# Kernel optimization log

Hardware: AMD Instinct MI355X
Metric: run time of the kernel (lower is better)

The kernel has to match this reference:

```python
import jax, jax.numpy as jnp
import numpy as np

EMBED_DIM = 1024
NUM_HEADS = 16
HEAD_DIM = EMBED_DIM // NUM_HEADS


def setup_inputs() -> dict:
    key = jax.random.key(0)
    ks = jax.random.split(key, 5)
    x = jax.random.normal(ks[0], (2, 2048, EMBED_DIM), dtype=jnp.float32)
    s_in = 1.0 / np.sqrt(EMBED_DIM)
    W_qkv = jax.random.uniform(ks[1], (EMBED_DIM, 3 * EMBED_DIM), minval=-s_in, maxval=s_in, dtype=jnp.float32)
    b_qkv = jax.random.uniform(ks[2], (3 * EMBED_DIM,), minval=-s_in, maxval=s_in, dtype=jnp.float32)
    W_out = jax.random.uniform(ks[3], (EMBED_DIM, EMBED_DIM), minval=-s_in, maxval=s_in, dtype=jnp.float32)
    b_out = jax.random.uniform(ks[4], (EMBED_DIM,), minval=-s_in, maxval=s_in, dtype=jnp.float32)
    return {"x": x, "W_qkv": W_qkv, "b_qkv": b_qkv, "W_out": W_out, "b_out": b_out}


def reference(x, W_qkv, b_qkv, W_out, b_out):
    B, S, D = x.shape
    H, Dh = NUM_HEADS, HEAD_DIM
    qkv = x @ W_qkv + b_qkv                       # [B, S, 3D]
    q, k, v = jnp.split(qkv, 3, axis=-1)
    # [B, S, D] -> [B, H, S, Dh]
    q = q.reshape(B, S, H, Dh).transpose(0, 2, 1, 3)
    k = k.reshape(B, S, H, Dh).transpose(0, 2, 1, 3)
    v = v.reshape(B, S, H, Dh).transpose(0, 2, 1, 3)
    scores = jnp.einsum('bhqd,bhkd->bhqk', q, k) / jnp.sqrt(jnp.float32(Dh))
    probs = jax.nn.softmax(scores, axis=-1)       # [B, H, S, S]
    attn = jnp.einsum('bhqk,bhkd->bhqd', probs, v)
    attn = attn.transpose(0, 2, 1, 3).reshape(B, S, D)
    return attn @ W_out + b_out
```

## Files before the change

kernel.cpp:

```cpp
#include <hip/hip_runtime.h>
#include <hip/hip_bf16.h>

#define DEV __device__ __forceinline__

typedef __bf16 bf16x8 __attribute__((ext_vector_type(8)));
typedef float f32x4 __attribute__((ext_vector_type(4)));
typedef float f32x16 __attribute__((ext_vector_type(16)));
using u16 = unsigned short;
using u32 = unsigned int;

static constexpr int S = 2048;
static constexpr int D = 1024;
static constexpr float SCQ = 0.125f * 1.44269504088896340736f;

DEV u16 f2bf(float f) {
  unsigned u = __builtin_bit_cast(unsigned, f);
  u += 0x7fffu + ((u >> 16) & 1u);
  return (u16)(u >> 16);
}
DEV u16 f2bfr(float f) {
  return (u16)((__builtin_bit_cast(u32, f) + 0x8000u) >> 16);
}
DEV u32 pk2(float a, float b) {
  u32 ua = __builtin_bit_cast(u32, a) + 0x8000u;
  u32 ub = __builtin_bit_cast(u32, b) + 0x8000u;
  return __builtin_amdgcn_perm(ub, ua, 0x07060302);
}

DEV void gl16(const u16* __restrict__ g, u16* l) {
  __builtin_amdgcn_global_load_lds((const __attribute__((address_space(1))) u32*)g,
                                   (__attribute__((address_space(3))) u32*)l, 16, 0, 0);
}

__global__ __launch_bounds__(256) void k_prep(const float* __restrict__ x, u16* __restrict__ Xb,
                                              const float* __restrict__ Wqkv, u16* __restrict__ WqkvT,
                                              const float* __restrict__ Wout, u16* __restrict__ WoutT) {
  __shared__ float t[32][33];
  const int bid = blockIdx.x;
  const int tid = threadIdx.x;
  if (bid < 4096) {
    const int i = bid * 256 + tid;
    const float4 v = reinterpret_cast<const float4*>(x)[i];
    ushort4 o;
    o.x = f2bf(v.x); o.y = f2bf(v.y); o.z = f2bf(v.z); o.w = f2bf(v.w);
    reinterpret_cast<ushort4*>(Xb)[i] = o;
    return;
  }
  const float* in;
  u16* out;
  int R, C, bx, by;
  if (bid < 4096 + 3072) {
    const int b = bid - 4096;
    in = Wqkv; out = WqkvT; R = 1024; C = 3072;
    bx = b % 96; by = b / 96;
  } else {
    const int b = bid - 7168;
    in = Wout; out = WoutT; R = 1024; C = 1024;
    bx = b & 31; by = b >> 5;
  }
  const int tx = tid & 31, ty = tid >> 5;
  const int c0 = bx * 32, r0 = by * 32;
  for (int i = ty; i < 32; i += 8)
    t[i][tx] = in[(size_t)(r0 + i) * C + c0 + tx];
  __syncthreads();
  for (int i = ty; i < 32; i += 8)
    out[(size_t)(c0 + i) * R + r0 + tx] = f2bf(t[tx][i]);
}

__global__ __launch_bounds__(256, 5) void k_gemm0(const u16* __restrict__ A, const u16* __restrict__ Bt,
                                                  const float* __restrict__ bias, int M, int N, int K,
                                                  u16* __restrict__ Qb, u16* __restrict__ Kb,
                                                  u16* __restrict__ Vt) {
  constexpr int TN = 128, NJ = 4;
  constexpr int ASZ = 2 * 128 * 32 * 2;
  __shared__ __align__(16) char smem[ASZ + 2 * TN * 32 * 2];
  auto As = reinterpret_cast<u16(*)[128][32]>(smem);
  auto Bs = reinterpret_cast<u16(*)[TN][32]>(smem + ASZ);
  auto LT = reinterpret_cast<u16(*)[136]>(smem);
  const int tid = threadIdx.x;
  const int lane = tid & 63, wave = tid >> 6;
  const int l15 = lane & 15, quad = lane >> 4;
  const int m0 = blockIdx.y * 128, n0 = blockIdx.x * TN;
  const int wm = (wave >> 1) * 64, wn = (wave & 1) * (TN / 2);
  const int lr = lane >> 2;
  const int lcs = ((((lane & 3) - (lane >> 3)) & 3)) * 8;
  const int sq = ((quad + (l15 >> 1)) & 3) * 8;

  f32x4 acc[4][NJ];
#pragma unroll
  for (int i = 0; i < 4; i++)
#pragma unroll
    for (int j = 0; j < NJ; j++) acc[i][j] = (f32x4){0.f, 0.f, 0.f, 0.f};

  const u16* Aw0 = &A[(size_t)(m0 + wave * 32 + lr) * K + lcs];
  const u16* Aw1 = &A[(size_t)(m0 + wave * 32 + 16 + lr) * K + lcs];
  const u16* Bw0 = &Bt[(size_t)(n0 + wave * 32 + lr) * K + lcs];
  const u16* Bw1 = &Bt[(size_t)(n0 + wave * 32 + 16 + lr) * K + lcs];

  gl16(Aw0, &As[0][wave * 32][0]);
  gl16(Aw1, &As[0][wave * 32 + 16][0]);
  gl16(Bw0, &Bs[0][wave * 32][0]);
  gl16(Bw1, &Bs[0][wave * 32 + 16][0]);

  int cur = 0;
#pragma unroll 2
  for (int kk = 0; kk < K; kk += 32, cur ^= 1) {
    __syncthreads();
    if (kk + 32 < K) {
      gl16(Aw0 + kk + 32, &As[cur ^ 1][wave * 32][0]);
      gl16(Aw1 + kk + 32, &As[cur ^ 1][wave * 32 + 16][0]);
      gl16(Bw0 + kk + 32, &Bs[cur ^ 1][wave * 32][0]);
      gl16(Bw1 + kk + 32, &Bs[cur ^ 1][wave * 32 + 16][0]);
    }
    bf16x8 af[4], bfv[NJ];
#pragma unroll
    for (int i = 0; i < 4; i++)
      af[i] = *reinterpret_cast<const bf16x8*>(&As[cur][wm + i * 16 + l15][sq]);
#pragma unroll
    for (int j = 0; j < NJ; j++)
      bfv[j] = *reinterpret_cast<const bf16x8*>(&Bs[cur][wn + j * 16 + l15][sq]);
#pragma unroll
    for (int i = 0; i < 4; i++)
#pragma unroll
      for (int j = 0; j < NJ; j++)
        acc[i][j] = __builtin_amdgcn_mfma_f32_16x16x32_bf16(af[i], bfv[j], acc[i][j], 0, 0, 0);
  }

  if (n0 >= 2048) {
    const int b = m0 >> 11, sbase = m0 & 2047;
#pragma unroll
    for (int p = 0; p < 2; p++) {
      __syncthreads();
      if ((wave & 1) == p) {
#pragma unroll
        for (int j = 0; j < NJ; j++) {
          const int n = n0 + wn + j * 16 + l15;
          const float vb = bias[n];
#pragma unroll
          for (int i = 0; i < 4; i++) {
            uint2 pw;
            pw.x = pk2(acc[i][j][0] + vb, acc[i][j][1] + vb);
            pw.y = pk2(acc[i][j][2] + vb, acc[i][j][3] + vb);
            *reinterpret_cast<uint2*>(&LT[j * 16 + l15][wm + i * 16 + quad * 4]) = pw;
          }
        }
      }
      __syncthreads();
      const int h = ((n0 - 2048) >> 6) + p;
      const int bh = b * 16 + h;
      const int nl = tid >> 2, cc = (tid & 3) * 32;
      u16* dst = &Vt[((size_t)bh * 64 + nl) * S + sbase + cc];
#pragma unroll
      for (int k = 0; k < 4; k++)
        reinterpret_cast<uint4*>(dst)[k] = *reinterpret_cast<const uint4*>(&LT[nl][cc + k * 8]);
    }
  } else {
#pragma unroll
    for (int i = 0; i < 4; i++) {
#pragma unroll
      for (int j = 0; j < NJ; j++) {
#pragma unroll
        for (int r = 0; r < 4; r++) {
          const int m = m0 + wm + i * 16 + quad * 4 + r;
          const int n = n0 + wn + j * 16 + l15;
          const float v = acc[i][j][r] + bias[n];
          const int h = (n >> 6) & 15, dh = n & 63;
          const int b = m >> 11, s = m & 2047;
          const int bh = b * 16 + h;
          if (n < 1024) Qb[((size_t)bh * S + s) * 64 + dh] = f2bfr(v * SCQ);
          else          Kb[((size_t)bh * S + s) * 64 + dh] = f2bfr(v);
        }
      }
    }
  }
}

__global__ __launch_bounds__(256, 4) void k_gemm2(const u16* __restrict__ A, const u16* __restrict__ Bt,
                                                  const float* __restrict__ bias, float* __restrict__ outF) {
  constexpr int K = 1024, N = 1024;
  __shared__ __align__(16) u16 As[2][64][64];
  __shared__ __align__(16) u16 Bs[2][64][64];
  const int tid = threadIdx.x;
  const int lane = tid & 63, wave = tid >> 6;
  const int l15 = lane & 15, quad = lane >> 4;
  const int m0 = blockIdx.y * 64, n0 = blockIdx.x * 64;
  const int wm = (wave >> 1) * 32, wn = (wave & 1) * 32;
  const int srow = lane >> 3;
  const int scol = ((lane & 7) ^ srow) * 8;

  f32x4 acc[2][2];
#pragma unroll
  for (int i = 0; i < 2; i++)
#pragma unroll
    for (int j = 0; j < 2; j++) acc[i][j] = (f32x4){0.f, 0.f, 0.f, 0.f};

  const u16* Ap[2];
  const u16* Bp[2];
#pragma unroll
  for (int c = 0; c < 2; c++) {
    Ap[c] = &A[(size_t)(m0 + wave * 16 + c * 8 + srow) * K + scol];
    Bp[c] = &Bt[(size_t)(n0 + wave * 16 + c * 8 + srow) * K + scol];
  }

#pragma unroll
  for (int c = 0; c < 2; c++) {
    gl16(Ap[c], &As[0][wave * 16 + c * 8][0]);
    gl16(Bp[c], &Bs[0][wave * 16 + c * 8][0]);
  }

  int cur = 0;
#pragma unroll 2
  for (int kk = 0; kk < K; kk += 64, cur ^= 1) {
    __syncthreads();
    if (kk + 64 < K) {
#pragma unroll
      for (int c = 0; c < 2; c++) {
        gl16(Ap[c] + kk + 64, &As[cur ^ 1][wave * 16 + c * 8][0]);
        gl16(Bp[c] + kk + 64, &Bs[cur ^ 1][wave * 16 + c * 8][0]);
      }
    }
#pragma unroll
    for (int ks = 0; ks < 2; ks++) {
      const int sc = ((ks * 4 + quad) ^ (l15 & 7)) * 8;
      bf16x8 af[2], bfv[2];
#pragma unroll
      for (int i = 0; i < 2; i++)
        af[i] = *reinterpret_cast<const bf16x8*>(&As[cur][wm + i * 16 + l15][sc]);
#pragma unroll
      for (int j = 0; j < 2; j++)
        bfv[j] = *reinterpret_cast<const bf16x8*>(&Bs[cur][wn + j * 16 + l15][sc]);
#pragma unroll
      for (int i = 0; i < 2; i++)
#pragma unroll
        for (int j = 0; j < 2; j++)
          acc[i][j] = __builtin_amdgcn_mfma_f32_16x16x32_bf16(af[i], bfv[j], acc[i][j], 0, 0, 0);
    }
  }

#pragma unroll
  for (int i = 0; i < 2; i++)
#pragma unroll
    for (int j = 0; j < 2; j++)
#pragma unroll
      for (int r = 0; r < 4; r++) {
        const int m = m0 + wm + i * 16 + quad * 4 + r;
        const int n = n0 + wn + j * 16 + l15;
        outF[(size_t)m * N + n] = acc[i][j][r] + bias[n];
      }
}

__global__ __launch_bounds__(256, 2) void k_attn(const u16* __restrict__ Qb,
                                                 const u16* __restrict__ Kb,
                                                 const u16* __restrict__ Vt,
                                                 u16* __restrict__ attnB) {
  __shared__ u16 Ks[64][72];
  __shared__ u16 Vs[64][72];
  __shared__ u16 Pl[4][32][72];
  const int bh = blockIdx.y;
  const int q0 = blockIdx.x * 128;
  const int tid = threadIdx.x;
  const int lane = tid & 63, wave = tid >> 6;
  const int l31 = lane & 31, hi = lane >> 5;
  const u16* Qh = Qb + (size_t)bh * S * 64;
  const u16* Kh = Kb + (size_t)bh * S * 64;
  const u16* Vh = Vt + (size_t)bh * 64 * S;
  const int qrow = q0 + wave * 32 + l31;
  bf16x8 qf[4];
#pragma unroll
  for (int f = 0; f < 4; f++)
    qf[f] = *reinterpret_cast<const bf16x8*>(&Qh[(size_t)qrow * 64 + f * 16 + hi * 8]);

  const int r0 = tid >> 3, c0 = (tid & 7) * 8;

  float li = 0.f;
  f32x16 o0, o1;
#pragma unroll
  for (int r = 0; r < 16; r++) { o0[r] = 0.f; o1[r] = 0.f; }

  uint4 pk0 = *reinterpret_cast<const uint4*>(&Kh[(size_t)r0 * 64 + c0]);
  uint4 pk1 = *reinterpret_cast<const uint4*>(&Kh[(size_t)(r0 + 32) * 64 + c0]);
  uint4 pv0 = *reinterpret_cast<const uint4*>(&Vh[(size_t)r0 * S + c0]);
  uint4 pv1 = *reinterpret_cast<const uint4*>(&Vh[(size_t)(r0 + 32) * S + c0]);

  for (int kb = 0; kb < S / 64; kb++) {
    __syncthreads();
    *reinterpret_cast<uint4*>(&Ks[r0][c0]) = pk0;
    *reinterpret_cast<uint4*>(&Ks[r0 + 32][c0]) = pk1;
    *reinterpret_cast<uint4*>(&Vs[r0][c0]) = pv0;
    *reinterpret_cast<uint4*>(&Vs[r0 + 32][c0]) = pv1;
    __syncthreads();
    if (kb + 1 < S / 64) {
      const u16* Kn = Kh + (size_t)(kb + 1) * 64 * 64;
      pk0 = *reinterpret_cast<const uint4*>(&Kn[(size_t)r0 * 64 + c0]);
      pk1 = *reinterpret_cast<const uint4*>(&Kn[(size_t)(r0 + 32) * 64 + c0]);
      pv0 = *reinterpret_cast<const uint4*>(&Vh[(size_t)r0 * S + (kb + 1) * 64 + c0]);
      pv1 = *reinterpret_cast<const uint4*>(&Vh[(size_t)(r0 + 32) * S + (kb + 1) * 64 + c0]);
    }
    f32x16 z[2];
    __builtin_amdgcn_s_setprio(1);
#pragma unroll
    for (int kt = 0; kt < 2; kt++) {
#pragma unroll
      for (int r = 0; r < 16; r++) z[kt][r] = 0.f;
#pragma unroll
      for (int f = 0; f < 4; f++) {
        const bf16x8 a = *reinterpret_cast<const bf16x8*>(&Ks[kt * 32 + l31][f * 16 + hi * 8]);
        z[kt] = __builtin_amdgcn_mfma_f32_32x32x16_bf16(a, qf[f], z[kt], 0, 0, 0);
      }
    }
    __builtin_amdgcn_s_setprio(0);
    float s0 = 0.f, s1 = 0.f, s2 = 0.f, s3 = 0.f;
#pragma unroll
    for (int kt = 0; kt < 2; kt++)
#pragma unroll
      for (int r = 0; r < 16; r++) {
        const float p = __builtin_amdgcn_exp2f(z[kt][r]);
        z[kt][r] = p;
        if ((r & 3) == 0) s0 += p; else if ((r & 3) == 1) s1 += p;
        else if ((r & 3) == 2) s2 += p; else s3 += p;
      }
    li += (s0 + s1) + (s2 + s3);
#pragma unroll
    for (int kt = 0; kt < 2; kt++)
#pragma unroll
      for (int g = 0; g < 4; g++) {
        uint2 pw;
        pw.x = pk2(z[kt][g * 4 + 0], z[kt][g * 4 + 1]);
        pw.y = pk2(z[kt][g * 4 + 2], z[kt][g * 4 + 3]);
        *reinterpret_cast<uint2*>(&Pl[wave][l31][kt * 32 + g * 8 + hi * 4]) = pw;
      }
    __builtin_amdgcn_s_setprio(1);
#pragma unroll
    for (int f = 0; f < 4; f++) {
      const bf16x8 bp = *reinterpret_cast<const bf16x8*>(&Pl[wave][l31][f * 16 + hi * 8]);
      const bf16x8 av0 = *reinterpret_cast<const bf16x8*>(&Vs[l31][f * 16 + hi * 8]);
      const bf16x8 av1 = *reinterpret_cast<const bf16x8*>(&Vs[32 + l31][f * 16 + hi * 8]);
      o0 = __builtin_amdgcn_mfma_f32_32x32x16_bf16(av0, bp, o0, 0, 0, 0);
      o1 = __builtin_amdgcn_mfma_f32_32x32x16_bf16(av1, bp, o1, 0, 0, 0);
    }
    __builtin_amdgcn_s_setprio(0);
  }
  li += __shfl_xor(li, 32);
  const float inv = 1.f / li;
#pragma unroll
  for (int dt = 0; dt < 2; dt++) {
    const f32x16& od = dt ? o1 : o0;
#pragma unroll
    for (int g = 0; g < 4; g++) {
      uint2 ow;
      ow.x = pk2(od[g * 4 + 0] * inv, od[g * 4 + 1] * inv);
      ow.y = pk2(od[g * 4 + 2] * inv, od[g * 4 + 3] * inv);
      *reinterpret_cast<uint2*>(&Pl[wave][l31][dt * 32 + g * 8 + hi * 4]) = ow;
    }
  }
  const int b = bh >> 4, h = bh & 15;
  const int mbase = b * S + q0 + wave * 32;
  const int qr = lane >> 1, ch = (lane & 1) * 32;
  u16* dst = &attnB[(size_t)(mbase + qr) * D + h * 64 + ch];
#pragma unroll
  for (int c = 0; c < 4; c++)
    reinterpret_cast<uint4*>(dst)[c] = *reinterpret_cast<const uint4*>(&Pl[wave][qr][ch + c * 8]);
}

extern "C" void kernel_launch(void* const* d_in, const int* in_sizes, int n_in,
                              void* d_out, int out_size, void* d_ws, size_t ws_size,
                              hipStream_t stream) {
  const float* x = (const float*)d_in[0];
  const float* Wqkv = (const float*)d_in[1];
  const float* bqkv = (const float*)d_in[2];
  const float* Wout = (const float*)d_in[3];
  const float* bout = (const float*)d_in[4];
  float* out = (float*)d_out;

  char* p = (char*)d_ws;
  u16* Xb = (u16*)p;    p += (size_t)4096 * 1024 * 2;
  u16* WqkvT = (u16*)p; p += (size_t)3072 * 1024 * 2;
  u16* WoutT = (u16*)p; p += (size_t)1024 * 1024 * 2;
  u16* Qb = (u16*)p;    p += (size_t)32 * 2048 * 64 * 2;
  u16* Kb = (u16*)p;    p += (size_t)32 * 2048 * 64 * 2;
  u16* Vt = (u16*)p;    p += (size_t)32 * 64 * 2048 * 2;
  u16* attnB = (u16*)p; p += (size_t)4096 * 1024 * 2;

  k_prep<<<4096 + 3072 + 1024, 256, 0, stream>>>(x, Xb, Wqkv, WqkvT, Wout, WoutT);
  k_gemm0<<<dim3(3072 / 128, 4096 / 128), 256, 0, stream>>>(
      Xb, WqkvT, bqkv, 4096, 3072, 1024, Qb, Kb, Vt);
  k_attn<<<dim3(2048 / 128, 32), 256, 0, stream>>>(Qb, Kb, Vt, attnB);
  k_gemm2<<<dim3(1024 / 64, 4096 / 64), 256, 0, stream>>>(attnB, WoutT, bout, out);
}
```

Before: 190.3 us.

## Double attention key tile to 128 and remap block order in GEMMs and attention

The attention kernel now processes 128 keys per iteration instead of 64, which halves the number of barrier-separated loop iterations and doubles the work per synchronisation. It uses larger shared-memory K, V and P tiles, and adds a barrier before the final output staging. All three kernels also remap the linear block id so that consecutive blocks are spread across groups of 8, intended to improve L2/cache locality across XCDs. The larger LDS footprint and higher register use may reduce occupancy in the attention kernel.

```diff
diff --git a/kernel.cpp b/kernel.cpp
--- a/kernel.cpp
+++ b/kernel.cpp
@@ -80,7 +80,9 @@
   const int tid = threadIdx.x;
   const int lane = tid & 63, wave = tid >> 6;
   const int l15 = lane & 15, quad = lane >> 4;
-  const int m0 = blockIdx.y * 128, n0 = blockIdx.x * TN;
+  const int bid0 = blockIdx.x + 24 * blockIdx.y;
+  const int bid = (bid0 & 7) * 96 + (bid0 >> 3);
+  const int m0 = (bid / 24) * 128, n0 = (bid % 24) * TN;
   const int wm = (wave >> 1) * 64, wn = (wave & 1) * (TN / 2);
   const int lr = lane >> 2;
   const int lcs = ((((lane & 3) - (lane >> 3)) & 3)) * 8;
@@ -183,7 +185,9 @@
   const int tid = threadIdx.x;
   const int lane = tid & 63, wave = tid >> 6;
   const int l15 = lane & 15, quad = lane >> 4;
-  const int m0 = blockIdx.y * 64, n0 = blockIdx.x * 64;
+  const int bid0 = blockIdx.x + 16 * blockIdx.y;
+  const int bid = (bid0 & 7) * 128 + (bid0 >> 3);
+  const int m0 = (bid >> 4) * 64, n0 = (bid & 15) * 64;
   const int wm = (wave >> 1) * 32, wn = (wave & 1) * 32;
   const int srow = lane >> 3;
   const int scol = ((lane & 7) ^ srow) * 8;
@@ -253,14 +257,16 @@
                                                  const u16* __restrict__ Kb,
                                                  const u16* __restrict__ Vt,
                                                  u16* __restrict__ attnB) {
-  __shared__ u16 Ks[64][72];
-  __shared__ u16 Vs[64][72];
-  __shared__ u16 Pl[4][32][72];
-  const int bh = blockIdx.y;
-  const int q0 = blockIdx.x * 128;
+  __shared__ u16 Ks[128][72];
+  __shared__ u16 Vs[64][136];
+  __shared__ u16 Pl[4][32][136];
   const int tid = threadIdx.x;
   const int lane = tid & 63, wave = tid >> 6;
   const int l31 = lane & 31, hi = lane >> 5;
+  const int bid0 = blockIdx.x + 16 * blockIdx.y;
+  const int bid = (bid0 & 7) * 64 + (bid0 >> 3);
+  const int bh = bid >> 4;
+  const int q0 = (bid & 15) * 128;
   const u16* Qh = Qb + (size_t)bh * S * 64;
   const u16* Kh = Kb + (size_t)bh * S * 64;
   const u16* Vh = Vt + (size_t)bh * 64 * S;
@@ -271,35 +277,41 @@
     qf[f] = *reinterpret_cast<const bf16x8*>(&Qh[(size_t)qrow * 64 + f * 16 + hi * 8]);
 
   const int r0 = tid >> 3, c0 = (tid & 7) * 8;
+  const int rv = tid >> 4, cv = (tid & 15) * 8;
 
   float li = 0.f;
   f32x16 o0, o1;
 #pragma unroll
   for (int r = 0; r < 16; r++) { o0[r] = 0.f; o1[r] = 0.f; }
 
-  uint4 pk0 = *reinterpret_cast<const uint4*>(&Kh[(size_t)r0 * 64 + c0]);
-  uint4 pk1 = *reinterpret_cast<const uint4*>(&Kh[(size_t)(r0 + 32) * 64 + c0]);
-  uint4 pv0 = *reinterpret_cast<const uint4*>(&Vh[(size_t)r0 * S + c0]);
-  uint4 pv1 = *reinterpret_cast<const uint4*>(&Vh[(size_t)(r0 + 32) * S + c0]);
-
-  for (int kb = 0; kb < S / 64; kb++) {
+  uint4 pk[4], pv[4];
+#pragma unroll
+  for (int c = 0; c < 4; c++) {
+    pk[c] = *reinterpret_cast<const uint4*>(&Kh[(size_t)(r0 + 32 * c) * 64 + c0]);
+    pv[c] = *reinterpret_cast<const uint4*>(&Vh[(size_t)(rv + 16 * c) * S + cv]);
+  }
+
+  for (int kb = 0; kb < S / 128; kb++) {
     __syncthreads();
-    *reinterpret_cast<uint4*>(&Ks[r0][c0]) = pk0;
-    *reinterpret_cast<uint4*>(&Ks[r0 + 32][c0]) = pk1;
-    *reinterpret_cast<uint4*>(&Vs[r0][c0]) = pv0;
-    *reinterpret_cast<uint4*>(&Vs[r0 + 32][c0]) = pv1;
+#pragma unroll
+    for (int c = 0; c < 4; c++) {
+      *reinterpret_cast<uint4*>(&Ks[r0 + 32 * c][c0]) = pk[c];
+      *reinterpret_cast<uint4*>(&Vs[rv + 16 * c][cv]) = pv[c];
+    }
     __syncthreads();
-    if (kb + 1 < S / 64) {
-      const u16* Kn = Kh + (size_t)(kb + 1) * 64 * 64;
-      pk0 = *reinterpret_cast<const uint4*>(&Kn[(size_t)r0 * 64 + c0]);
-      pk1 = *reinterpret_cast<const uint4*>(&Kn[(size_t)(r0 + 32) * 64 + c0]);
-      pv0 = *reinterpret_cast<const uint4*>(&Vh[(size_t)r0 * S + (kb + 1) * 64 + c0]);
-      pv1 = *reinterpret_cast<const uint4*>(&Vh[(size_t)(r0 + 32) * S + (kb + 1) * 64 + c0]);
-    }
-    f32x16 z[2];
+    if (kb + 1 < S / 128) {
+      const u16* Kn = Kh + (size_t)(kb + 1) * 128 * 64;
+      const u16* Vn = Vh + (size_t)(kb + 1) * 128;
+#pragma unroll
+      for (int c = 0; c < 4; c++) {
+        pk[c] = *reinterpret_cast<const uint4*>(&Kn[(size_t)(r0 + 32 * c) * 64 + c0]);
+        pv[c] = *reinterpret_cast<const uint4*>(&Vn[(size_t)(rv + 16 * c) * S + cv]);
+      }
+    }
+    f32x16 z[4];
     __builtin_amdgcn_s_setprio(1);
 #pragma unroll
-    for (int kt = 0; kt < 2; kt++) {
+    for (int kt = 0; kt < 4; kt++) {
 #pragma unroll
       for (int r = 0; r < 16; r++) z[kt][r] = 0.f;
 #pragma unroll
@@ -311,7 +323,7 @@
     __builtin_amdgcn_s_setprio(0);
     float s0 = 0.f, s1 = 0.f, s2 = 0.f, s3 = 0.f;
 #pragma unroll
-    for (int kt = 0; kt < 2; kt++)
+    for (int kt = 0; kt < 4; kt++)
 #pragma unroll
       for (int r = 0; r < 16; r++) {
         const float p = __builtin_amdgcn_exp2f(z[kt][r]);
@@ -321,7 +333,7 @@
       }
     li += (s0 + s1) + (s2 + s3);
 #pragma unroll
-    for (int kt = 0; kt < 2; kt++)
+    for (int kt = 0; kt < 4; kt++)
 #pragma unroll
       for (int g = 0; g < 4; g++) {
         uint2 pw;
@@ -331,7 +343,7 @@
       }
     __builtin_amdgcn_s_setprio(1);
 #pragma unroll
-    for (int f = 0; f < 4; f++) {
+    for (int f = 0; f < 8; f++) {
       const bf16x8 bp = *reinterpret_cast<const bf16x8*>(&Pl[wave][l31][f * 16 + hi * 8]);
       const bf16x8 av0 = *reinterpret_cast<const bf16x8*>(&Vs[l31][f * 16 + hi * 8]);
       const bf16x8 av1 = *reinterpret_cast<const bf16x8*>(&Vs[32 + l31][f * 16 + hi * 8]);
@@ -353,6 +365,7 @@
       *reinterpret_cast<uint2*>(&Pl[wave][l31][dt * 32 + g * 8 + hi * 4]) = ow;
     }
   }
+  __syncthreads();
   const int b = bh >> 4, h = bh & 15;
   const int mbase = b * S + q0 + wave * 32;
   const int qr = lane >> 1, ch = (lane & 1) * 32;
```

Result: slower. 235.9 us (+24.0%).
